# Optimization experiments

Measured on AMD Instinct MI355X. Metric: run time of the kernel, lower is better.

The kernel has to match this reference:

```python
import jax, jax.numpy as jnp
import numpy as np

IN, OUT, RANK, ORDER, BATCH = 1024, 1024, 32, 3, 4096


def setup_inputs() -> dict:
    key = jax.random.key(0)
    ks = jax.random.split(key, 16)
    inp = {}
    inp['X'] = jax.random.normal(ks[0], (BATCH, IN), dtype=jnp.float32)
    inp['const'] = jnp.zeros((OUT,), dtype=jnp.float32)
    for i in range(ORDER):
        # Taylor-style scales: keep magnitudes controlled for higher orders
        o_std = (1.0 / RANK) ** 0.5 if i == 0 else 0.01
        inp[f'O{i}'] = o_std * jax.random.normal(ks[1 + i], (OUT, RANK), dtype=jnp.float32)
        base = 1.0
        for t in range(i + 1):
            base = base / (RANK + 2 * t)
        i_std = base ** (1.0 / 2 ** (i + 1))
        inp[f'I{i}'] = i_std * jax.random.normal(ks[4 + i], (i + 1, RANK, IN), dtype=jnp.float32)
        g_std = (1.0 / RANK ** (i + 1)) ** 0.5
        inp[f'G{i}'] = g_std * jax.random.normal(ks[7 + i], (RANK, RANK ** (i + 1)), dtype=jnp.float32)
    return inp


def _taylor_forward(X, const, Os, Is, Gs):
    # X: (batch, in). X0 = 0.0 so no shift needed beyond subtracting 0.
    batch = X.shape[0]
    rank = Is[0].shape[1]
    Y = jnp.broadcast_to(const[None, :], (batch, const.shape[0]))
    for i in range(len(Os)):
        # Z[j] = I[j] @ X.T -> (i+1, rank, batch)
        Z = jnp.einsum('jri,bi->jrb', Is[i], X)
        kron = Z[0]  # (rank, batch)
        for j in range(1, i + 1):
            # broadcasted outer product, matching torch loop order:
            # result[z_j, z_{j-1}, ..., z_0, batch]
            X3 = Z[j].reshape((rank,) + (1,) * j + (batch,))
            kron = kron[None] * X3
        kron = kron.reshape((-1, batch))  # (rank**(i+1), batch)
        Y = Y + (Os[i] @ (Gs[i] @ kron)).T
    return Y


def reference(X, const, O0, O1, O2, I0, I1, I2, G0, G1, G2):
    return _taylor_forward(X, const, [O0, O1, O2], [I0, I1, I2], [G0, G1, G2])
```

## Files before the change

### kernel.cpp

```cpp
#include <hip/hip_runtime.h>


typedef float f4 __attribute__((ext_vector_type(4)));
typedef _Float16 h8 __attribute__((ext_vector_type(8)));
typedef _Float16 h4 __attribute__((ext_vector_type(4)));
typedef unsigned int u32x4 __attribute__((ext_vector_type(4)));

#define ZH_OFF  0u
#define TH_OFF  1572864u
#define OCH_OFF 2097152u
#define G2H_OFF 2293760u

__device__ __forceinline__ h8 splat8(unsigned int u) {
    _Float16 s = __builtin_bit_cast(_Float16, (unsigned short)(u & 0xffffu));
    return h8{ s, s, s, s, s, s, s, s };
}

__device__ __forceinline__ void stage_bcast16(const _Float16* zsrc, unsigned int* dst) {
    u32x4 u0 = *(const u32x4*)zsrc;
    u32x4 u1 = *(const u32x4*)(zsrc + 8);
    #pragma unroll
    for (int k = 0; k < 4; ++k) {
        dst[2*k]       = (u0[k] & 0xffffu) * 0x00010001u;
        dst[2*k + 1]   = (u0[k] >> 16)     * 0x00010001u;
        dst[8 + 2*k]   = (u1[k] & 0xffffu) * 0x00010001u;
        dst[8 + 2*k+1] = (u1[k] >> 16)     * 0x00010001u;
    }
}

__global__ __launch_bounds__(256) void prep_gemmx(
    const float* __restrict__ X,
    const float* __restrict__ I0, const float* __restrict__ I1, const float* __restrict__ I2,
    const float* __restrict__ O0, const float* __restrict__ O1, const float* __restrict__ O2,
    const float* __restrict__ G0, const float* __restrict__ G2,
    _Float16* __restrict__ Och, _Float16* __restrict__ G2h, _Float16* __restrict__ Z)
{
    const int bx = blockIdx.x;
    const int t = threadIdx.x;
    if (bx >= 192) {
        if (bx < 1216) {
            int i = ((bx - 192) * 256 + t) * 4;
            f4 v = *(const f4*)(G2 + i);
            h4 o = { (_Float16)v[0], (_Float16)v[1], (_Float16)v[2], (_Float16)v[3] };
            *(h4*)(G2h + i) = o;
        } else {
            int idx = (bx - 1216) * 256 + t;
            int o = idx / 96, j = idx - o * 96;
            float v;
            if (j < 32) {
                v = 0.f;
                #pragma unroll
                for (int q = 0; q < 32; ++q) v += O0[o*32 + q] * G0[q*32 + j];
            } else if (j < 64) v = O1[o*32 + (j - 32)];
            else               v = O2[o*32 + (j - 64)];
            Och[idx] = (_Float16)v;
        }
        return;
    }
    __shared__ _Float16 As[2][64 * 64];
    __shared__ _Float16 Bs[2][64 * 64];
    const int work = (bx & 7) * 24 + (bx >> 3);
    const int m0 = (work / 3) * 64, n0 = (work % 3) * 64;
    const int wid = t >> 6, lane = t & 63;
    const int wr = wid >> 1, wc = wid & 1;
    const int lr = lane & 15, lg = lane >> 4;
    const int arow = t >> 2, aq = t & 3;

    const float* xbase = X + (size_t)(m0 + arow) * 1024 + aq * 16;
    const int wrow = n0 + arow;
    const float* wbase = (wrow < 32) ? I0 + (size_t)wrow * 1024
                       : (wrow < 96) ? I1 + (size_t)(wrow - 32) * 1024
                                     : I2 + (size_t)(wrow - 96) * 1024;
    wbase += aq * 16;
    const int sw0 = arow * 64 + (((aq * 2)     ^ (arow & 7)) << 3);
    const int sw1 = arow * 64 + (((aq * 2 + 1) ^ (arow & 7)) << 3);

    f4 xa[2][4], wa[2][4];
    #define LOADX(set, step) { \
        const float* xp = xbase + (step) * 64; \
        const float* wp = wbase + (step) * 64; \
        _Pragma("unroll") \
        for (int q = 0; q < 4; ++q) { xa[set][q] = *(const f4*)(xp + q*4); wa[set][q] = *(const f4*)(wp + q*4); } }
    #define STAGE(set, buf) { \
        h8 ha0, ha1, hb0, hb1; \
        _Pragma("unroll") \
        for (int j = 0; j < 4; ++j) { \
            ha0[j] = (_Float16)xa[set][0][j]; ha0[4+j] = (_Float16)xa[set][1][j]; \
            ha1[j] = (_Float16)xa[set][2][j]; ha1[4+j] = (_Float16)xa[set][3][j]; \
            hb0[j] = (_Float16)wa[set][0][j]; hb0[4+j] = (_Float16)wa[set][1][j]; \
            hb1[j] = (_Float16)wa[set][2][j]; hb1[4+j] = (_Float16)wa[set][3][j]; \
        } \
        *(h8*)&As[buf][sw0] = ha0; *(h8*)&As[buf][sw1] = ha1; \
        *(h8*)&Bs[buf][sw0] = hb0; *(h8*)&Bs[buf][sw1] = hb1; }

    LOADX(0, 0); LOADX(1, 1);
    STAGE(0, 0);
    LOADX(0, 2);

    f4 acc[2][2];
    #pragma unroll
    for (int mt = 0; mt < 2; ++mt)
        #pragma unroll
        for (int nt = 0; nt < 2; ++nt) acc[mt][nt] = f4{0.f,0.f,0.f,0.f};

    #pragma unroll
    for (int s = 0; s < 16; ++s) {
        const int cur = s & 1;
        __syncthreads();
        if (s < 15) STAGE((s + 1) & 1, cur ^ 1);
        if (s < 13) LOADX((s + 1) & 1, s + 3);
        #pragma unroll
        for (int ks = 0; ks < 2; ++ks) {
            h8 av[2], bv[2];
            #pragma unroll
            for (int mt = 0; mt < 2; ++mt) {
                int row = wr * 32 + mt * 16 + lr, gg = ks * 4 + lg;
                av[mt] = *(const h8*)&As[cur][row * 64 + ((gg ^ (row & 7)) << 3)];
            }
            #pragma unroll
            for (int nt = 0; nt < 2; ++nt) {
                int row = wc * 32 + nt * 16 + lr, gg = ks * 4 + lg;
                bv[nt] = *(const h8*)&Bs[cur][row * 64 + ((gg ^ (row & 7)) << 3)];
            }
            #pragma unroll
            for (int mt = 0; mt < 2; ++mt)
                #pragma unroll
                for (int nt = 0; nt < 2; ++nt)
                    acc[mt][nt] = __builtin_amdgcn_mfma_f32_16x16x32_f16(av[mt], bv[nt], acc[mt][nt], 0, 0, 0);
        }
    }
    #undef LOADX
    #undef STAGE
    #pragma unroll
    for (int mt = 0; mt < 2; ++mt)
        #pragma unroll
        for (int nt = 0; nt < 2; ++nt)
            #pragma unroll
            for (int i = 0; i < 4; ++i)
                Z[(size_t)(m0 + wr*32 + mt*16 + lg*4 + i) * 192 + n0 + wc*32 + nt*16 + lr]
                    = (_Float16)acc[mt][nt][i];
}

__global__ __launch_bounds__(256) void kron_fused(
    const _Float16* __restrict__ Z, const _Float16* __restrict__ G2h,
    const float* __restrict__ G1, _Float16* __restrict__ T)
{
    __shared__ __align__(16) unsigned char smem[37376];
    unsigned int* Zs1 = (unsigned int*)smem;
    _Float16* Bs = (_Float16*)(smem + 16896);
    const int bx = blockIdx.x;
    const int t = threadIdx.x;
    const int wid = t >> 6, lane = t & 63;
    const int lr = lane & 15, lg = lane >> 4;
    const bool is_t2 = bx < 512;
    const int m0 = is_t2 ? (bx >> 4) * 128 : (bx - 512) * 128;
    const int zcol = is_t2 ? 128 : 64;

    {
        int row = t >> 1, c0 = (t & 1) * 16;
        stage_bcast16(Z + (size_t)(m0 + row) * 192 + zcol + c0, Zs1 + row * 33 + c0);
    }

    if (is_t2) {
        const int n0 = (bx & 15) * 64;
        const int wm0 = (wid >> 1) * 64, wn0 = (wid & 1) * 32;
        h8 a0v[4];
        #pragma unroll
        for (int mt = 0; mt < 4; ++mt)
            a0v[mt] = *(const h8*)(Z + (size_t)(m0 + wm0 + mt*16 + lr) * 192 + 96 + lg * 8);

        f4 acc[4][2];
        #pragma unroll
        for (int mt = 0; mt < 4; ++mt)
            #pragma unroll
            for (int nt = 0; nt < 2; ++nt) acc[mt][nt] = f4{0.f, 0.f, 0.f, 0.f};

        const int brow = t >> 2, bg = t & 3;
        const f4* gsrc = (const f4*)(G2h + (size_t)(n0 + brow) * 1024 + bg * 8);
        f4 brA[2], brB[2];
        brA[0] = gsrc[0];  brB[0] = gsrc[4];
        {
            *(f4*)&Bs[0 * 5120 + 0 * 2560 + brow * 40 + bg * 8] = brA[0];
            *(f4*)&Bs[0 * 5120 + 1 * 2560 + brow * 40 + bg * 8] = brB[0];
        }
        brA[1] = gsrc[8];  brB[1] = gsrc[12];
        brA[0] = gsrc[16]; brB[0] = gsrc[20];

        unsigned int zu[2][2][4];
        #pragma unroll
        for (int i = 0; i < 16; ++i) {
            const int cur = i & 1;
            __syncthreads();
            if (i == 0) {
                #pragma unroll
                for (int q = 0; q < 2; ++q)
                    #pragma unroll
                    for (int mt = 0; mt < 4; ++mt)
                        zu[0][q][mt] = Zs1[(wm0 + mt*16 + lr) * 33 + q];
            }
            if (i < 15) {
                const int set = (i + 1) & 1;
                *(f4*)&Bs[(cur ^ 1) * 5120 + 0 * 2560 + brow * 40 + bg * 8] = brA[set];
                *(f4*)&Bs[(cur ^ 1) * 5120 + 1 * 2560 + brow * 40 + bg * 8] = brB[set];
                #pragma unroll
                for (int q = 0; q < 2; ++q)
                    #pragma unroll
                    for (int mt = 0; mt < 4; ++mt)
                        zu[set][q][mt] = Zs1[(wm0 + mt*16 + lr) * 33 + 2*(i+1) + q];
            }
            if (i < 13) {
                const int set = (i + 1) & 1;
                brA[set] = gsrc[(i + 3) * 8];
                brB[set] = gsrc[(i + 3) * 8 + 4];
            }
            #pragma unroll
            for (int q = 0; q < 2; ++q) {
                h8 bf0 = *(const h8*)&Bs[cur * 5120 + q * 2560 + (wn0 + lr) * 40 + lg * 8];
                h8 bf1 = *(const h8*)&Bs[cur * 5120 + q * 2560 + (wn0 + 16 + lr) * 40 + lg * 8];
                #pragma unroll
                for (int mt = 0; mt < 4; ++mt) {
                    h8 z1b = splat8(zu[cur][q][mt]);
                    h8 af = z1b * a0v[mt];
                    acc[mt][0] = __builtin_amdgcn_mfma_f32_16x16x32_f16(af, bf0, acc[mt][0], 0, 0, 0);
                    acc[mt][1] = __builtin_amdgcn_mfma_f32_16x16x32_f16(af, bf1, acc[mt][1], 0, 0, 0);
                }
            }
        }

        __syncthreads();
        float* Ms = (float*)smem;
        #pragma unroll
        for (int mt = 0; mt < 4; ++mt)
            #pragma unroll
            for (int nt = 0; nt < 2; ++nt)
                #pragma unroll
                for (int i = 0; i < 4; ++i)
                    Ms[(wm0 + mt*16 + lg*4 + i) * 66 + wn0 + nt*16 + lr] = acc[mt][nt][i];
        __syncthreads();
        {
            int row = t >> 1, rl = t & 1;
            const _Float16* z2p = Z + (size_t)(m0 + row) * 192 + 160;
            const float* mrow = Ms + row * 66 + rl * 32;
            float sum = 0.f;
            #pragma unroll
            for (int r2 = 0; r2 < 32; ++r2) sum += mrow[r2] * (float)z2p[r2];
            T[(size_t)(m0 + row) * 64 + 32 + (bx & 15) * 2 + rl] = (_Float16)sum;
        }
    } else {
        h8 a0v[2];
        #pragma unroll
        for (int mt = 0; mt < 2; ++mt)
            a0v[mt] = *(const h8*)(Z + (size_t)(m0 + wid*32 + mt*16 + lr) * 192 + 32 + lg * 8);

        const int brow = t >> 3, bq = (t & 7) * 4;
        const float* g1src = G1 + (size_t)brow * 1024 + bq;
        f4 bw = *(const f4*)g1src;
        {
            h4 bh = { (_Float16)bw[0], (_Float16)bw[1], (_Float16)bw[2], (_Float16)bw[3] };
            *(h4*)&Bs[brow * 40 + bq] = bh;
        }
        bw = *(const f4*)(g1src + 32);

        f4 acc[2][2];
        #pragma unroll
        for (int mt = 0; mt < 2; ++mt)
            #pragma unroll
            for (int nt = 0; nt < 2; ++nt) acc[mt][nt] = f4{0.f,0.f,0.f,0.f};
        __syncthreads();

        for (int s = 0; s < 32; ++s) {
            const int cur = s & 1;
            if (s < 31) {
                h4 bh = { (_Float16)bw[0], (_Float16)bw[1], (_Float16)bw[2], (_Float16)bw[3] };
                *(h4*)&Bs[(cur ^ 1) * 1280 + brow * 40 + bq] = bh;
            }
            if (s < 30) bw = *(const f4*)(g1src + (s + 2) * 32);
            h8 bf[2];
            #pragma unroll
            for (int nt = 0; nt < 2; ++nt)
                bf[nt] = *(const h8*)&Bs[cur * 1280 + (nt*16 + lr) * 40 + lg * 8];
            #pragma unroll
            for (int mt = 0; mt < 2; ++mt) {
                h8 z1b = splat8(Zs1[(wid*32 + mt*16 + lr) * 33 + s]);
                h8 af = z1b * a0v[mt];
                acc[mt][0] = __builtin_amdgcn_mfma_f32_16x16x32_f16(af, bf[0], acc[mt][0], 0, 0, 0);
                acc[mt][1] = __builtin_amdgcn_mfma_f32_16x16x32_f16(af, bf[1], acc[mt][1], 0, 0, 0);
            }
            __syncthreads();
        }
        #pragma unroll
        for (int mt = 0; mt < 2; ++mt)
            #pragma unroll
            for (int nt = 0; nt < 2; ++nt)
                #pragma unroll
                for (int i = 0; i < 4; ++i)
                    T[(size_t)(m0 + wid*32 + mt*16 + lg*4 + i) * 64 + nt*16 + lr]
                        = (_Float16)acc[mt][nt][i];
    }
}

__global__ __launch_bounds__(256) void gemm_y_mfma(
    const _Float16* __restrict__ Z, const _Float16* __restrict__ T,
    const _Float16* __restrict__ Och, const float* __restrict__ cst,
    float* __restrict__ Y)
{
    __shared__ _Float16 As[64 * 104];
    __shared__ _Float16 Bs[128 * 104];
    const int t = threadIdx.x;
    const int n0 = blockIdx.x * 128, m0 = blockIdx.y * 64;
    {
        int row = t >> 2, seg = t & 3;
        const _Float16* zp = Z + (size_t)(m0 + row) * 192;
        const _Float16* tp = T + (size_t)(m0 + row) * 64;
        _Float16* dst = As + row * 104;
        if (seg == 0) {
            *(h8*)(dst)      = *(const h8*)(zp);
            *(h8*)(dst + 8)  = *(const h8*)(zp + 8);
            *(h8*)(dst + 16) = *(const h8*)(zp + 16);
        } else if (seg == 1) {
            *(h8*)(dst + 24) = *(const h8*)(zp + 24);
            *(h8*)(dst + 32) = *(const h8*)(tp);
            *(h8*)(dst + 40) = *(const h8*)(tp + 8);
        } else if (seg == 2) {
            *(h8*)(dst + 48) = *(const h8*)(tp + 16);
            *(h8*)(dst + 56) = *(const h8*)(tp + 24);
            *(h8*)(dst + 64) = *(const h8*)(tp + 32);
        } else {
            *(h8*)(dst + 72) = *(const h8*)(tp + 40);
            *(h8*)(dst + 80) = *(const h8*)(tp + 48);
            *(h8*)(dst + 88) = *(const h8*)(tp + 56);
        }
        int row2 = t >> 1, half = t & 1;
        const _Float16* src = Och + (size_t)(n0 + row2) * 96 + half * 48;
        _Float16* bdst = Bs + row2 * 104 + half * 48;
        #pragma unroll
        for (int q = 0; q < 6; ++q) *(h8*)(bdst + q * 8) = *(const h8*)(src + q * 8);
    }
    const int wid = t >> 6, lane = t & 63;
    const int wvr = wid >> 1, wvc = wid & 1;
    const int lr = lane & 15, lg = lane >> 4;
    float bias[4];
    #pragma unroll
    for (int nt = 0; nt < 4; ++nt) bias[nt] = cst[n0 + wvc*64 + nt*16 + lr];
    __syncthreads();

    f4 acc[2][4];
    #pragma unroll
    for (int mt = 0; mt < 2; ++mt)
        #pragma unroll
        for (int nt = 0; nt < 4; ++nt) acc[mt][nt] = f4{0.f,0.f,0.f,0.f};

    #pragma unroll
    for (int ks = 0; ks < 3; ++ks) {
        h8 av[2], bv[4];
        #pragma unroll
        for (int mt = 0; mt < 2; ++mt)
            av[mt] = *(const h8*)&As[(wvr*32 + mt*16 + lr) * 104 + ks*32 + lg*8];
        #pragma unroll
        for (int nt = 0; nt < 4; ++nt)
            bv[nt] = *(const h8*)&Bs[(wvc*64 + nt*16 + lr) * 104 + ks*32 + lg*8];
        #pragma unroll
        for (int mt = 0; mt < 2; ++mt)
            #pragma unroll
            for (int nt = 0; nt < 4; ++nt)
                acc[mt][nt] = __builtin_amdgcn_mfma_f32_16x16x32_f16(av[mt], bv[nt], acc[mt][nt], 0, 0, 0);
    }
    #pragma unroll
    for (int mt = 0; mt < 2; ++mt)
        #pragma unroll
        for (int nt = 0; nt < 4; ++nt)
            #pragma unroll
            for (int i = 0; i < 4; ++i)
                Y[(size_t)(m0 + wvr*32 + mt*16 + lg*4 + i) * 1024 + n0 + wvc*64 + nt*16 + lr]
                    = acc[mt][nt][i] + bias[nt];
}

extern "C" void kernel_launch(void* const* d_in, const int* in_sizes, int n_in,
                              void* d_out, int out_size, void* d_ws, size_t ws_size,
                              hipStream_t stream) {
    const float* X   = (const float*)d_in[0];
    const float* cst = (const float*)d_in[1];
    const float* O0  = (const float*)d_in[2];
    const float* I0  = (const float*)d_in[3];
    const float* G0  = (const float*)d_in[4];
    const float* O1  = (const float*)d_in[5];
    const float* I1  = (const float*)d_in[6];
    const float* G1  = (const float*)d_in[7];
    const float* O2  = (const float*)d_in[8];
    const float* I2  = (const float*)d_in[9];
    const float* G2  = (const float*)d_in[10];
    unsigned char* ws = (unsigned char*)d_ws;
    _Float16* Zh  = (_Float16*)(ws + ZH_OFF);
    _Float16* Th  = (_Float16*)(ws + TH_OFF);
    _Float16* Oh  = (_Float16*)(ws + OCH_OFF);
    _Float16* G2h = (_Float16*)(ws + G2H_OFF);
    float* Y = (float*)d_out;

    prep_gemmx<<<1600, 256, 0, stream>>>(X, I0, I1, I2, O0, O1, O2, G0, G2, Oh, G2h, Zh);
    kron_fused<<<544, 256, 0, stream>>>(Zh, G2h, G1, Th);
    gemm_y_mfma<<<dim3(8, 64), 256, 0, stream>>>(Zh, Th, Oh, cst, Y);
}
```

Before: 39.30 us.

## Split K across two thread groups in prep GEMM with LDS reduction

The X·I GEMM blocks now use 512 threads. Each group of 256 handles half of the K dimension (512 of 1024), and the partial accumulators are combined through shared memory before the fp16 store. With only 192 GEMM tiles, this is meant to halve the serial K loop per block and raise in-flight memory traffic. The side conversion blocks are regridded to match the new thread count. The cost is doubled LDS per block, an extra reduction pass with two barriers, and fewer resident blocks per CU.

```diff
diff --git a/kernel.cpp b/kernel.cpp
--- a/kernel.cpp
+++ b/kernel.cpp
@@ -28,7 +28,7 @@
     }
 }
 
-__global__ __launch_bounds__(256) void prep_gemmx(
+__global__ __launch_bounds__(512) void prep_gemmx(
     const float* __restrict__ X,
     const float* __restrict__ I0, const float* __restrict__ I1, const float* __restrict__ I2,
     const float* __restrict__ O0, const float* __restrict__ O1, const float* __restrict__ O2,
@@ -38,13 +38,13 @@
     const int bx = blockIdx.x;
     const int t = threadIdx.x;
     if (bx >= 192) {
-        if (bx < 1216) {
-            int i = ((bx - 192) * 256 + t) * 4;
+        if (bx < 704) {
+            int i = ((bx - 192) * 512 + t) * 4;
             f4 v = *(const f4*)(G2 + i);
             h4 o = { (_Float16)v[0], (_Float16)v[1], (_Float16)v[2], (_Float16)v[3] };
             *(h4*)(G2h + i) = o;
         } else {
-            int idx = (bx - 1216) * 256 + t;
+            int idx = (bx - 704) * 512 + t;
             int o = idx / 96, j = idx - o * 96;
             float v;
             if (j < 32) {
@@ -57,21 +57,23 @@
         }
         return;
     }
-    __shared__ _Float16 As[2][64 * 64];
-    __shared__ _Float16 Bs[2][64 * 64];
+    __shared__ _Float16 As[2][2][64 * 64];
+    __shared__ _Float16 Bs[2][2][64 * 64];
+    const int g  = t >> 8;
+    const int tt = t & 255;
     const int work = (bx & 7) * 24 + (bx >> 3);
     const int m0 = (work / 3) * 64, n0 = (work % 3) * 64;
-    const int wid = t >> 6, lane = t & 63;
+    const int wid = tt >> 6, lane = tt & 63;
     const int wr = wid >> 1, wc = wid & 1;
     const int lr = lane & 15, lg = lane >> 4;
-    const int arow = t >> 2, aq = t & 3;
-
-    const float* xbase = X + (size_t)(m0 + arow) * 1024 + aq * 16;
+    const int arow = tt >> 2, aq = tt & 3;
+
+    const float* xbase = X + (size_t)(m0 + arow) * 1024 + g * 512 + aq * 16;
     const int wrow = n0 + arow;
     const float* wbase = (wrow < 32) ? I0 + (size_t)wrow * 1024
                        : (wrow < 96) ? I1 + (size_t)(wrow - 32) * 1024
                                      : I2 + (size_t)(wrow - 96) * 1024;
-    wbase += aq * 16;
+    wbase += g * 512 + aq * 16;
     const int sw0 = arow * 64 + (((aq * 2)     ^ (arow & 7)) << 3);
     const int sw1 = arow * 64 + (((aq * 2 + 1) ^ (arow & 7)) << 3);
 
@@ -90,8 +92,8 @@
             hb0[j] = (_Float16)wa[set][0][j]; hb0[4+j] = (_Float16)wa[set][1][j]; \
             hb1[j] = (_Float16)wa[set][2][j]; hb1[4+j] = (_Float16)wa[set][3][j]; \
         } \
-        *(h8*)&As[buf][sw0] = ha0; *(h8*)&As[buf][sw1] = ha1; \
-        *(h8*)&Bs[buf][sw0] = hb0; *(h8*)&Bs[buf][sw1] = hb1; }
+        *(h8*)&As[g][buf][sw0] = ha0; *(h8*)&As[g][buf][sw1] = ha1; \
+        *(h8*)&Bs[g][buf][sw0] = hb0; *(h8*)&Bs[g][buf][sw1] = hb1; }
 
     LOADX(0, 0); LOADX(1, 1);
     STAGE(0, 0);
@@ -104,23 +106,23 @@
         for (int nt = 0; nt < 2; ++nt) acc[mt][nt] = f4{0.f,0.f,0.f,0.f};
 
     #pragma unroll
-    for (int s = 0; s < 16; ++s) {
+    for (int s = 0; s < 8; ++s) {
         const int cur = s & 1;
         __syncthreads();
-        if (s < 15) STAGE((s + 1) & 1, cur ^ 1);
-        if (s < 13) LOADX((s + 1) & 1, s + 3);
+        if (s < 7) STAGE((s + 1) & 1, cur ^ 1);
+        if (s < 5) LOADX((s + 1) & 1, s + 3);
         #pragma unroll
         for (int ks = 0; ks < 2; ++ks) {
             h8 av[2], bv[2];
             #pragma unroll
             for (int mt = 0; mt < 2; ++mt) {
                 int row = wr * 32 + mt * 16 + lr, gg = ks * 4 + lg;
-                av[mt] = *(const h8*)&As[cur][row * 64 + ((gg ^ (row & 7)) << 3)];
+                av[mt] = *(const h8*)&As[g][cur][row * 64 + ((gg ^ (row & 7)) << 3)];
             }
             #pragma unroll
             for (int nt = 0; nt < 2; ++nt) {
                 int row = wc * 32 + nt * 16 + lr, gg = ks * 4 + lg;
-                bv[nt] = *(const h8*)&Bs[cur][row * 64 + ((gg ^ (row & 7)) << 3)];
+                bv[nt] = *(const h8*)&Bs[g][cur][row * 64 + ((gg ^ (row & 7)) << 3)];
             }
             #pragma unroll
             for (int mt = 0; mt < 2; ++mt)
@@ -131,14 +133,28 @@
     }
     #undef LOADX
     #undef STAGE
-    #pragma unroll
-    for (int mt = 0; mt < 2; ++mt)
-        #pragma unroll
-        for (int nt = 0; nt < 2; ++nt)
-            #pragma unroll
-            for (int i = 0; i < 4; ++i)
-                Z[(size_t)(m0 + wr*32 + mt*16 + lg*4 + i) * 192 + n0 + wc*32 + nt*16 + lr]
-                    = (_Float16)acc[mt][nt][i];
+    __syncthreads();
+    float* Red = (float*)&As[0][0][0];
+    if (g == 1) {
+        #pragma unroll
+        for (int mt = 0; mt < 2; ++mt)
+            #pragma unroll
+            for (int nt = 0; nt < 2; ++nt)
+                #pragma unroll
+                for (int i = 0; i < 4; ++i)
+                    Red[tt * 16 + mt * 8 + nt * 4 + i] = acc[mt][nt][i];
+    }
+    __syncthreads();
+    if (g == 0) {
+        #pragma unroll
+        for (int mt = 0; mt < 2; ++mt)
+            #pragma unroll
+            for (int nt = 0; nt < 2; ++nt)
+                #pragma unroll
+                for (int i = 0; i < 4; ++i)
+                    Z[(size_t)(m0 + wr*32 + mt*16 + lg*4 + i) * 192 + n0 + wc*32 + nt*16 + lr]
+                        = (_Float16)(acc[mt][nt][i] + Red[tt * 16 + mt * 8 + nt * 4 + i]);
+    }
 }
 
 __global__ __launch_bounds__(256) void kron_fused(
@@ -396,7 +412,7 @@
     _Float16* G2h = (_Float16*)(ws + G2H_OFF);
     float* Y = (float*)d_out;
 
-    prep_gemmx<<<1600, 256, 0, stream>>>(X, I0, I1, I2, O0, O1, O2, G0, G2, Oh, G2h, Zh);
+    prep_gemmx<<<896, 512, 0, stream>>>(X, I0, I1, I2, O0, O1, O2, G0, G2, Oh, G2h, Zh);
     kron_fused<<<544, 256, 0, stream>>>(Zh, G2h, G1, Th);
     gemm_y_mfma<<<dim3(8, 64), 256, 0, stream>>>(Zh, Th, Oh, cst, Y);
 }
```

After: 36.52 us, median of 3. 7.1% less time.
